# Kernel optimization log

Measured on AMD Instinct MI355X. Metric: run time of the kernel, lower is better.

## Reference

```python
import jax, jax.numpy as jnp
import numpy as np

T = 128
IN_SIZE = 1024
OUT_SIZE = 1024
LMBDA = 0.01          # lmbda_in_in (also used for out_in update, as in source)
MAX_POST = 1.0
MAX_PRE = 1.0
CONN_SPARSITY = 0.1   # in_in_sparsity / out_in_sparsity


def setup_inputs() -> dict:
    key = jax.random.key(0)
    k1, k2, k3, k4, k5 = jax.random.split(key, 5)
    inputs = jax.random.normal(k1, (T, IN_SIZE), dtype=jnp.float32)
    # fixed weights ~ nn.Linear init (uniform +-1/sqrt(fan_in)) * g * sparse mask
    b_in = 1.0 / np.sqrt(IN_SIZE)
    in_in_fixed = jax.random.uniform(k2, (IN_SIZE, IN_SIZE), jnp.float32, -b_in, b_in)
    in_in_fixed = in_in_fixed * (jax.random.uniform(k3, (IN_SIZE, IN_SIZE)) < CONN_SPARSITY).astype(jnp.float32)
    b_out = 1.0 / np.sqrt(IN_SIZE)
    out_in_fixed = jax.random.uniform(k4, (OUT_SIZE, IN_SIZE), jnp.float32, -b_out, b_out)
    out_in_fixed = out_in_fixed * (jax.random.uniform(k5, (OUT_SIZE, IN_SIZE)) < CONN_SPARSITY).astype(jnp.float32)
    return {"inputs": inputs, "in_in_fixed": in_in_fixed, "out_in_fixed": out_in_fixed}


def _renorm(P, max_post, max_pre):
    # row (post) renorm then column (pre) renorm, only where sums exceed cap
    post = P.sum(axis=1)
    P = P * jnp.where(post > max_post, max_post / post, 1.0)[:, None]
    pre = P.sum(axis=0)
    P = P * jnp.where(pre > max_pre, max_pre / pre, 1.0)[None, :]
    return P


def reference(inputs, in_in_fixed, out_in_fixed):
    def step(carry, x):
        in_in_p, out_in_p = carry
        # forward_input path: out = F.linear(in_, out_in)
        out = (out_in_fixed + out_in_p) @ x                      # [OUT_SIZE]
        # Hebbian outer-product updates + renorm homeostasis
        in_in_p = _renorm(in_in_p + LMBDA * jnp.outer(x, x), MAX_POST, MAX_PRE)
        out_in_p = _renorm(out_in_p + LMBDA * jnp.outer(out, x), MAX_POST, MAX_PRE)
        return (in_in_p, out_in_p), out

    init = (jnp.zeros_like(in_in_fixed), jnp.zeros_like(out_in_fixed))
    (in_in_p, out_in_p), outs = jax.lax.scan(step, init, inputs)
    return outs  # [T, OUT_SIZE]
```

## Files before the change

kernel.cpp:

```cpp
#include <hip/hip_runtime.h>


typedef float f32x4 __attribute__((ext_vector_type(4)));
typedef float f32x2 __attribute__((ext_vector_type(2)));

#define T_STEPS 128
#define N 1024
#define GR 16
#define GC 16
#define TB 64
#define NT 256
#define LMBDA 0.01f

__global__ __launch_bounds__(NT) void rf2d_kernel(
    const float* __restrict__ X,
    const float* __restrict__ W,
    float* __restrict__ OUT,
    f32x4* __restrict__ OutA,
    f32x2* __restrict__ ScolB,
    unsigned* __restrict__ fAr,
    unsigned* __restrict__ fBc) {
  __shared__ float Pl[TB * TB];
  __shared__ float f_loc[TB];
  __shared__ float rfl[TB], rol_l[TB];
  __shared__ float SLc[4][TB];
  __shared__ float SLd[4][TB];
  __shared__ float sxAll[T_STEPS];

  const int tid = threadIdx.x;
  const int b = blockIdx.x;
  const int r = b >> 4, c = b & 15;
  const int grow = r * TB, gcol = c * TB;
  const int r_loc = tid >> 2, q = tid & 3;
  const int c_loc = tid & 63, rg = tid >> 6;

  for (int i = tid; i < TB * TB; i += NT) Pl[i] = 0.f;
  if (tid < TB) f_loc[tid] = 1.f;
  if (tid < T_STEPS) {
    const f32x4* X4i = (const f32x4*)(X + (size_t)tid * N);
    f32x4 acc = {0.f, 0.f, 0.f, 0.f};
    for (int j = 0; j < N / 4; ++j) acc += X4i[j];
    sxAll[tid] = (acc.x + acc.y) + (acc.z + acc.w);
  }
  f32x4 wr[4];
#pragma unroll
  for (int k = 0; k < 4; ++k)
    wr[k] = *(const f32x4*)(W + (size_t)(grow + r_loc) * N + gcol + 16 * q + 4 * k);

  float wrx = 0.f;
  {
    const f32x4* Xn = (const f32x4*)(X + gcol);
#pragma unroll
    for (int k = 0; k < 4; ++k) {
      f32x4 xv = Xn[4 * q + k];
      wrx += (wr[k].x * xv.x + wr[k].y * xv.y) + (wr[k].z * xv.z + wr[k].w * xv.w);
    }
  }
  __syncthreads();

  for (int t = 0; t < T_STEPS; ++t) {
    const int p = t & 1;
    const unsigned tg = t + 1u;
    const float tagf = __uint_as_float(tg);

    float a_out = wrx, a_R = 0.f;
    {
      f32x4* PlV = (f32x4*)Pl;
      const f32x4* FV = (const f32x4*)f_loc;
      const f32x4* XV = (const f32x4*)(X + (size_t)t * N + gcol);
#pragma unroll
      for (int k = 0; k < 4; ++k) {
        const int lc = 4 * q + k;
        const int slot = r_loc * 16 + (lc ^ (r_loc & 15));
        f32x4 pv = PlV[slot];
        f32x4 fv = FV[lc];
        f32x4 xv = XV[lc];
        f32x4 pf = pv * fv;
        PlV[slot] = pf;
        a_R += (pf.x + pf.y) + (pf.z + pf.w);
        a_out += (pf.x * xv.x + pf.y * xv.y) + (pf.z * xv.z + pf.w * xv.w);
      }
    }
    a_out += __shfl_xor(a_out, 1, 64); a_out += __shfl_xor(a_out, 2, 64);
    a_R   += __shfl_xor(a_R, 1, 64);   a_R   += __shfl_xor(a_R, 2, 64);

    if (q == 0) {
      f32x4 v; v.x = a_out; v.y = a_R; v.z = tagf; v.w = 0.f;
      f32x4* dst = OutA + (size_t)p * GC * N + (size_t)c * N + grow + r_loc;
      asm volatile("global_store_dwordx4 %0, %1, off sc0 sc1"
                   :: "v"(dst), "v"(v) : "memory");
    }

    f32x4 v0, v1, v2, v3;
    {
      const f32x4* baseA = OutA + (size_t)p * GC * N + grow + r_loc;
      for (;;) {
        asm volatile("global_load_dwordx4 %0, %4, off sc0 sc1\n\t"
                     "global_load_dwordx4 %1, %5, off sc0 sc1\n\t"
                     "global_load_dwordx4 %2, %6, off sc0 sc1\n\t"
                     "global_load_dwordx4 %3, %7, off sc0 sc1\n\t"
                     "s_waitcnt vmcnt(0)"
                     : "=v"(v0), "=v"(v1), "=v"(v2), "=v"(v3)
                     : "v"(baseA + (size_t)(4 * q + 0) * N),
                       "v"(baseA + (size_t)(4 * q + 1) * N),
                       "v"(baseA + (size_t)(4 * q + 2) * N),
                       "v"(baseA + (size_t)(4 * q + 3) * N)
                     : "memory");
        __builtin_amdgcn_sched_barrier(0);
        if (__float_as_uint(v0.z) == tg && __float_as_uint(v1.z) == tg &&
            __float_as_uint(v2.z) == tg && __float_as_uint(v3.z) == tg)
          break;
      }
    }
    {
      float po = (v0.x + v1.x) + (v2.x + v3.x);
      float pR = (v0.y + v1.y) + (v2.y + v3.y);
      po += __shfl_xor(po, 1, 64); po += __shfl_xor(po, 2, 64);
      pR += __shfl_xor(pR, 1, 64); pR += __shfl_xor(pR, 2, 64);
      float ol = LMBDA * po;
      float R1 = pR + ol * sxAll[t];
      float rf = (R1 > 1.f) ? 1.f / R1 : 1.f;
      if (q == 0) { rfl[r_loc] = rf; rol_l[r_loc] = rf * ol; }
      if (c == 0 && q == 0) OUT[(size_t)t * N + grow + r_loc] = po;
    }
    if (t == T_STEPS - 1) break;
    __syncthreads();

    if (tid == 0)
      __hip_atomic_store(&fAr[r * GC + c], tg, __ATOMIC_RELAXED, __HIP_MEMORY_SCOPE_AGENT);

    {
      const float xc = X[(size_t)t * N + gcol + c_loc];
      float cacc = 0.f;
#pragma unroll
      for (int rr = 0; rr < 16; ++rr) {
        const int row = rg * 16 + rr;
        const int idx = row * 64 + ((((c_loc >> 2) ^ (row & 15))) << 2) + (c_loc & 3);
        float v = rfl[row] * Pl[idx] + rol_l[row] * xc;
        Pl[idx] = v;
        cacc += v;
      }
      SLc[rg][c_loc] = cacc;
    }
    if (tid < 16 && (int)t >= 2) {
      const unsigned tgt = t - 1u;
      while (__hip_atomic_load(&fBc[c * GR + tid], __ATOMIC_RELAXED,
                               __HIP_MEMORY_SCOPE_AGENT) < tgt)
        __builtin_amdgcn_s_sleep(1);
    }
    __syncthreads();

    if (tid < TB) {
      float scol = (SLc[0][tid] + SLc[1][tid]) + (SLc[2][tid] + SLc[3][tid]);
      f32x2 v; v.x = scol; v.y = tagf;
      f32x2* dst = ScolB + (size_t)p * GR * N + (size_t)r * N + gcol + tid;
      asm volatile("global_store_dwordx2 %0, %1, off sc0 sc1"
                   :: "v"(dst), "v"(v) : "memory");
    }

    wrx = 0.f;
    {
      const f32x4* Xn = (const f32x4*)(X + (size_t)(t + 1) * N + gcol);
#pragma unroll
      for (int k = 0; k < 4; ++k) {
        f32x4 xv = Xn[4 * q + k];
        wrx += (wr[k].x * xv.x + wr[k].y * xv.y) + (wr[k].z * xv.z + wr[k].w * xv.w);
      }
    }

    {
      f32x2 u0, u1, u2, u3;
      const f32x2* baseB = ScolB + (size_t)p * GR * N + gcol + c_loc;
      for (;;) {
        asm volatile("global_load_dwordx2 %0, %4, off sc0 sc1\n\t"
                     "global_load_dwordx2 %1, %5, off sc0 sc1\n\t"
                     "global_load_dwordx2 %2, %6, off sc0 sc1\n\t"
                     "global_load_dwordx2 %3, %7, off sc0 sc1\n\t"
                     "s_waitcnt vmcnt(0)"
                     : "=v"(u0), "=v"(u1), "=v"(u2), "=v"(u3)
                     : "v"(baseB + (size_t)(4 * rg + 0) * N),
                       "v"(baseB + (size_t)(4 * rg + 1) * N),
                       "v"(baseB + (size_t)(4 * rg + 2) * N),
                       "v"(baseB + (size_t)(4 * rg + 3) * N)
                     : "memory");
        __builtin_amdgcn_sched_barrier(0);
        if (__float_as_uint(u0.y) == tg && __float_as_uint(u1.y) == tg &&
            __float_as_uint(u2.y) == tg && __float_as_uint(u3.y) == tg)
          break;
      }
      SLd[rg][c_loc] = (u0.x + u1.x) + (u2.x + u3.x);
    }
    __syncthreads();

    if (tid == 0)
      __hip_atomic_store(&fBc[c * GR + r], tg, __ATOMIC_RELAXED, __HIP_MEMORY_SCOPE_AGENT);
    if (tid < TB) {
      float s = (SLd[0][tid] + SLd[1][tid]) + (SLd[2][tid] + SLd[3][tid]);
      f_loc[tid] = (s > 1.f) ? 1.f / s : 1.f;
    }
    if (tid >= 16 && tid < 32 && t >= 1) {
      const unsigned tgt = t;
      while (__hip_atomic_load(&fAr[r * GC + (tid - 16)], __ATOMIC_RELAXED,
                               __HIP_MEMORY_SCOPE_AGENT) < tgt)
        __builtin_amdgcn_s_sleep(1);
    }
    __syncthreads();
  }
}

extern "C" void kernel_launch(void* const* d_in, const int* in_sizes, int n_in,
                              void* d_out, int out_size, void* d_ws, size_t ws_size,
                              hipStream_t stream) {
  const float* X = (const float*)d_in[0];
  const float* W = (const float*)d_in[2];
  float* OUT = (float*)d_out;

  char* ws = (char*)d_ws;
  unsigned* fAr = (unsigned*)ws;
  unsigned* fBc = (unsigned*)(ws + 1024);
  f32x4* OutA = (f32x4*)(ws + 4096);
  f32x2* ScolB = (f32x2*)(ws + 4096 + (size_t)2 * GC * N * sizeof(f32x4));

  hipMemsetAsync(ws, 0, 2048, stream);

  hipLaunchKernelGGL(rf2d_kernel, dim3(GR * GC), dim3(NT), 0, stream,
                     X, W, OUT, OutA, ScolB, fAr, fBc);
}
```

Measured before the change: 743.7 us.

## Replace tagged-payload polling with per-block flag arrays for cross-block exchange

After: 632.0 us. 15.0% less time.

```diff
diff --git a/kernel.cpp b/kernel.cpp
--- a/kernel.cpp
+++ b/kernel.cpp
@@ -3,6 +3,7 @@
 
 typedef float f32x4 __attribute__((ext_vector_type(4)));
 typedef float f32x2 __attribute__((ext_vector_type(2)));
+typedef unsigned u32x4 __attribute__((ext_vector_type(4)));
 
 #define T_STEPS 128
 #define N 1024
@@ -16,10 +17,12 @@
     const float* __restrict__ X,
     const float* __restrict__ W,
     float* __restrict__ OUT,
-    f32x4* __restrict__ OutA,
-    f32x2* __restrict__ ScolB,
+    f32x2* __restrict__ OutP,
+    float* __restrict__ Scol,
     unsigned* __restrict__ fAr,
-    unsigned* __restrict__ fBc) {
+    unsigned* __restrict__ fAc,
+    unsigned* __restrict__ fBc,
+    unsigned* __restrict__ fBr) {
   __shared__ float Pl[TB * TB];
   __shared__ float f_loc[TB];
   __shared__ float rfl[TB], rol_l[TB];
@@ -36,12 +39,17 @@
 
   for (int i = tid; i < TB * TB; i += NT) Pl[i] = 0.f;
   if (tid < TB) f_loc[tid] = 1.f;
-  if (tid < T_STEPS) {
-    const f32x4* X4i = (const f32x4*)(X + (size_t)tid * N);
+  {
+    const int rowi = tid >> 1, half = tid & 1;
+    const f32x4* Xr = (const f32x4*)(X + (size_t)rowi * N) + half * 128;
     f32x4 acc = {0.f, 0.f, 0.f, 0.f};
-    for (int j = 0; j < N / 4; ++j) acc += X4i[j];
-    sxAll[tid] = (acc.x + acc.y) + (acc.z + acc.w);
+    for (int j = 0; j < 128; ++j) acc += Xr[j];
+    ((float*)SLc)[tid] = (acc.x + acc.y) + (acc.z + acc.w);
   }
+  __syncthreads();
+  if (tid < T_STEPS)
+    sxAll[tid] = ((float*)SLc)[2 * tid] + ((float*)SLc)[2 * tid + 1];
+
   f32x4 wr[4];
 #pragma unroll
   for (int k = 0; k < 4; ++k)
@@ -61,7 +69,6 @@
   for (int t = 0; t < T_STEPS; ++t) {
     const int p = t & 1;
     const unsigned tg = t + 1u;
-    const float tagf = __uint_as_float(tg);
 
     float a_out = wrx, a_R = 0.f;
     {
@@ -85,34 +92,43 @@
     a_R   += __shfl_xor(a_R, 1, 64);   a_R   += __shfl_xor(a_R, 2, 64);
 
     if (q == 0) {
-      f32x4 v; v.x = a_out; v.y = a_R; v.z = tagf; v.w = 0.f;
-      f32x4* dst = OutA + (size_t)p * GC * N + (size_t)c * N + grow + r_loc;
-      asm volatile("global_store_dwordx4 %0, %1, off sc0 sc1"
+      f32x2 v; v.x = a_out; v.y = a_R;
+      f32x2* dst = OutP + (size_t)p * GC * N + (size_t)c * N + grow + r_loc;
+      asm volatile("global_store_dwordx2 %0, %1, off sc0 sc1"
                    :: "v"(dst), "v"(v) : "memory");
     }
-
-    f32x4 v0, v1, v2, v3;
-    {
-      const f32x4* baseA = OutA + (size_t)p * GC * N + grow + r_loc;
+    __syncthreads();
+    if (tid == 0) {
+      __hip_atomic_store(&fAr[r * GC + c], tg, __ATOMIC_RELAXED, __HIP_MEMORY_SCOPE_AGENT);
+      __hip_atomic_store(&fAc[c * GR + r], tg, __ATOMIC_RELAXED, __HIP_MEMORY_SCOPE_AGENT);
+    }
+
+    {
+      const unsigned* fp = fAr + r * GC + 4 * q;
+      u32x4 fv;
       for (;;) {
-        asm volatile("global_load_dwordx4 %0, %4, off sc0 sc1\n\t"
-                     "global_load_dwordx4 %1, %5, off sc0 sc1\n\t"
-                     "global_load_dwordx4 %2, %6, off sc0 sc1\n\t"
-                     "global_load_dwordx4 %3, %7, off sc0 sc1\n\t"
-                     "s_waitcnt vmcnt(0)"
-                     : "=v"(v0), "=v"(v1), "=v"(v2), "=v"(v3)
-                     : "v"(baseA + (size_t)(4 * q + 0) * N),
-                       "v"(baseA + (size_t)(4 * q + 1) * N),
-                       "v"(baseA + (size_t)(4 * q + 2) * N),
-                       "v"(baseA + (size_t)(4 * q + 3) * N)
-                     : "memory");
+        asm volatile("global_load_dwordx4 %0, %1, off sc0 sc1\n\ts_waitcnt vmcnt(0)"
+                     : "=v"(fv) : "v"(fp) : "memory");
         __builtin_amdgcn_sched_barrier(0);
-        if (__float_as_uint(v0.z) == tg && __float_as_uint(v1.z) == tg &&
-            __float_as_uint(v2.z) == tg && __float_as_uint(v3.z) == tg)
-          break;
-      }
-    }
-    {
+        if (fv.x >= tg && fv.y >= tg && fv.z >= tg && fv.w >= tg) break;
+        __builtin_amdgcn_s_sleep(1);
+      }
+    }
+    {
+      f32x2 v0, v1, v2, v3;
+      const f32x2* baseA = OutP + (size_t)p * GC * N + grow + r_loc;
+      asm volatile("global_load_dwordx2 %0, %4, off sc0 sc1\n\t"
+                   "global_load_dwordx2 %1, %5, off sc0 sc1\n\t"
+                   "global_load_dwordx2 %2, %6, off sc0 sc1\n\t"
+                   "global_load_dwordx2 %3, %7, off sc0 sc1\n\t"
+                   "s_waitcnt vmcnt(0)"
+                   : "=v"(v0), "=v"(v1), "=v"(v2), "=v"(v3)
+                   : "v"(baseA + (size_t)(4 * q + 0) * N),
+                     "v"(baseA + (size_t)(4 * q + 1) * N),
+                     "v"(baseA + (size_t)(4 * q + 2) * N),
+                     "v"(baseA + (size_t)(4 * q + 3) * N)
+                   : "memory");
+      __builtin_amdgcn_sched_barrier(0);
       float po = (v0.x + v1.x) + (v2.x + v3.x);
       float pR = (v0.y + v1.y) + (v2.y + v3.y);
       po += __shfl_xor(po, 1, 64); po += __shfl_xor(po, 2, 64);
@@ -126,9 +142,6 @@
     if (t == T_STEPS - 1) break;
     __syncthreads();
 
-    if (tid == 0)
-      __hip_atomic_store(&fAr[r * GC + c], tg, __ATOMIC_RELAXED, __HIP_MEMORY_SCOPE_AGENT);
-
     {
       const float xc = X[(size_t)t * N + gcol + c_loc];
       float cacc = 0.f;
@@ -142,20 +155,23 @@
       }
       SLc[rg][c_loc] = cacc;
     }
-    if (tid < 16 && (int)t >= 2) {
-      const unsigned tgt = t - 1u;
-      while (__hip_atomic_load(&fBc[c * GR + tid], __ATOMIC_RELAXED,
-                               __HIP_MEMORY_SCOPE_AGENT) < tgt)
+    if (tid < 16) {
+      while (__hip_atomic_load(&fAc[c * GR + tid], __ATOMIC_RELAXED,
+                               __HIP_MEMORY_SCOPE_AGENT) < tg)
         __builtin_amdgcn_s_sleep(1);
     }
     __syncthreads();
 
     if (tid < TB) {
       float scol = (SLc[0][tid] + SLc[1][tid]) + (SLc[2][tid] + SLc[3][tid]);
-      f32x2 v; v.x = scol; v.y = tagf;
-      f32x2* dst = ScolB + (size_t)p * GR * N + (size_t)r * N + gcol + tid;
-      asm volatile("global_store_dwordx2 %0, %1, off sc0 sc1"
-                   :: "v"(dst), "v"(v) : "memory");
+      float* dst = Scol + (size_t)p * GR * N + (size_t)r * N + gcol + tid;
+      asm volatile("global_store_dword %0, %1, off sc0 sc1"
+                   :: "v"(dst), "v"(scol) : "memory");
+    }
+    __syncthreads();
+    if (tid == 0) {
+      __hip_atomic_store(&fBc[c * GR + r], tg, __ATOMIC_RELAXED, __HIP_MEMORY_SCOPE_AGENT);
+      __hip_atomic_store(&fBr[r * GC + c], tg, __ATOMIC_RELAXED, __HIP_MEMORY_SCOPE_AGENT);
     }
 
     wrx = 0.f;
@@ -169,40 +185,42 @@
     }
 
     {
-      f32x2 u0, u1, u2, u3;
-      const f32x2* baseB = ScolB + (size_t)p * GR * N + gcol + c_loc;
+      const unsigned* fp = fBc + c * GR + 4 * rg;
+      u32x4 fv;
       for (;;) {
-        asm volatile("global_load_dwordx2 %0, %4, off sc0 sc1\n\t"
-                     "global_load_dwordx2 %1, %5, off sc0 sc1\n\t"
-                     "global_load_dwordx2 %2, %6, off sc0 sc1\n\t"
-                     "global_load_dwordx2 %3, %7, off sc0 sc1\n\t"
-                     "s_waitcnt vmcnt(0)"
-                     : "=v"(u0), "=v"(u1), "=v"(u2), "=v"(u3)
-                     : "v"(baseB + (size_t)(4 * rg + 0) * N),
-                       "v"(baseB + (size_t)(4 * rg + 1) * N),
-                       "v"(baseB + (size_t)(4 * rg + 2) * N),
-                       "v"(baseB + (size_t)(4 * rg + 3) * N)
-                     : "memory");
+        asm volatile("global_load_dwordx4 %0, %1, off sc0 sc1\n\ts_waitcnt vmcnt(0)"
+                     : "=v"(fv) : "v"(fp) : "memory");
         __builtin_amdgcn_sched_barrier(0);
-        if (__float_as_uint(u0.y) == tg && __float_as_uint(u1.y) == tg &&
-            __float_as_uint(u2.y) == tg && __float_as_uint(u3.y) == tg)
-          break;
-      }
-      SLd[rg][c_loc] = (u0.x + u1.x) + (u2.x + u3.x);
-    }
-    __syncthreads();
-
-    if (tid == 0)
-      __hip_atomic_store(&fBc[c * GR + r], tg, __ATOMIC_RELAXED, __HIP_MEMORY_SCOPE_AGENT);
+        if (fv.x >= tg && fv.y >= tg && fv.z >= tg && fv.w >= tg) break;
+        __builtin_amdgcn_s_sleep(1);
+      }
+    }
+    {
+      float u0, u1, u2, u3;
+      const float* baseB = Scol + (size_t)p * GR * N + gcol + c_loc;
+      asm volatile("global_load_dword %0, %4, off sc0 sc1\n\t"
+                   "global_load_dword %1, %5, off sc0 sc1\n\t"
+                   "global_load_dword %2, %6, off sc0 sc1\n\t"
+                   "global_load_dword %3, %7, off sc0 sc1\n\t"
+                   "s_waitcnt vmcnt(0)"
+                   : "=v"(u0), "=v"(u1), "=v"(u2), "=v"(u3)
+                   : "v"(baseB + (size_t)(4 * rg + 0) * N),
+                     "v"(baseB + (size_t)(4 * rg + 1) * N),
+                     "v"(baseB + (size_t)(4 * rg + 2) * N),
+                     "v"(baseB + (size_t)(4 * rg + 3) * N)
+                   : "memory");
+      __builtin_amdgcn_sched_barrier(0);
+      SLd[rg][c_loc] = (u0 + u1) + (u2 + u3);
+    }
+    if (tid >= 16 && tid < 32) {
+      while (__hip_atomic_load(&fBr[r * GC + (tid - 16)], __ATOMIC_RELAXED,
+                               __HIP_MEMORY_SCOPE_AGENT) < tg)
+        __builtin_amdgcn_s_sleep(1);
+    }
+    __syncthreads();
     if (tid < TB) {
       float s = (SLd[0][tid] + SLd[1][tid]) + (SLd[2][tid] + SLd[3][tid]);
       f_loc[tid] = (s > 1.f) ? 1.f / s : 1.f;
-    }
-    if (tid >= 16 && tid < 32 && t >= 1) {
-      const unsigned tgt = t;
-      while (__hip_atomic_load(&fAr[r * GC + (tid - 16)], __ATOMIC_RELAXED,
-                               __HIP_MEMORY_SCOPE_AGENT) < tgt)
-        __builtin_amdgcn_s_sleep(1);
     }
     __syncthreads();
   }
@@ -217,12 +235,14 @@
 
   char* ws = (char*)d_ws;
   unsigned* fAr = (unsigned*)ws;
-  unsigned* fBc = (unsigned*)(ws + 1024);
-  f32x4* OutA = (f32x4*)(ws + 4096);
-  f32x2* ScolB = (f32x2*)(ws + 4096 + (size_t)2 * GC * N * sizeof(f32x4));
-
-  hipMemsetAsync(ws, 0, 2048, stream);
+  unsigned* fAc = (unsigned*)(ws + 1024);
+  unsigned* fBc = (unsigned*)(ws + 2048);
+  unsigned* fBr = (unsigned*)(ws + 3072);
+  f32x2* OutP = (f32x2*)(ws + 4096);
+  float* Scol = (float*)(ws + 4096 + (size_t)2 * GC * N * sizeof(f32x2));
+
+  hipMemsetAsync(ws, 0, 4096, stream);
 
   hipLaunchKernelGGL(rf2d_kernel, dim3(GR * GC), dim3(NT), 0, stream,
-                     X, W, OUT, OutA, ScolB, fAr, fBc);
+                     X, W, OUT, OutP, Scol, fAr, fAc, fBc, fBr);
 }
```
